# Kernel tuning notes

Hardware: AMD Instinct MI355X
Metric: run time of the kernel (lower is better)

The kernel has to match this reference:

```python
import jax, jax.numpy as jnp
import numpy as np

NUM_SINK = 8  # cfg.SINKHORN_ITERS


def _sinkhorn_log(c, log_a, log_b, lambd):
    # c: [M+1, N+1] augmented coupling scores (sinkhorn_unrolled: log_p = -c/lambd)
    log_p = -c / lambd
    for _ in range(NUM_SINK):  # fixed small unroll, matches num_sink
        log_p = log_p - (jax.nn.logsumexp(log_p, axis=-2, keepdims=True) - log_b[None, :])
        log_p = log_p - (jax.nn.logsumexp(log_p, axis=-1, keepdims=True) - log_a[:, None])
    return jnp.exp(log_p)


def setup_inputs() -> dict:
    key = jax.random.key(0)
    k1, k2 = jax.random.split(key)
    G, M, N, D = 128, 512, 512, 512
    return {
        "det_feats": jax.random.normal(k1, (G, N, D), dtype=jnp.float32),
        "tra_feats": jax.random.normal(k2, (G, M, D), dtype=jnp.float32),
        "alpha": jnp.ones((1,), dtype=jnp.float32),
        "eplison": jnp.zeros((1,), dtype=jnp.float32),
    }


def reference(det_feats, tra_feats, alpha, eplison):
    G, N, D = det_feats.shape
    M = tra_feats.shape[1]
    # cosine affinity per graph: [G, M, N]
    corr = jnp.einsum('gmd,gnd->gmn', tra_feats, det_feats)
    n1 = jnp.linalg.norm(tra_feats, axis=-1)  # [G, M]
    n2 = jnp.linalg.norm(det_feats, axis=-1)  # [G, N]
    affinity = corr / (n1[:, :, None] * n2[:, None, :])
    a = alpha[0]
    bins0 = jnp.broadcast_to(a, (G, M, 1)).astype(affinity.dtype)
    bins1 = jnp.broadcast_to(a, (G, 1, N)).astype(affinity.dtype)
    corner = jnp.broadcast_to(a, (G, 1, 1)).astype(affinity.dtype)
    couplings = jnp.concatenate([
        jnp.concatenate([affinity, bins0], axis=-1),
        jnp.concatenate([bins1, corner], axis=-1),
    ], axis=-2)  # [G, M+1, N+1]
    norm = 1.0 / (M + N)
    a_aug = jnp.full((M + 1,), norm, dtype=jnp.float32).at[-1].set(norm * N)
    b_aug = jnp.full((N + 1,), norm, dtype=jnp.float32).at[-1].set(norm * M)
    log_a = jnp.log(a_aug)
    log_b = jnp.log(b_aug)
    lambd = jnp.exp(eplison[0]) + 0.03
    pred = jax.vmap(lambda c: _sinkhorn_log(c, log_a, log_b, lambd))(couplings)
    return pred  # [G, M+1, N+1]
```

## Files before the change

kernel.cpp:

```cpp
#include <hip/hip_runtime.h>
#include <hip/hip_bf16.h>

#define G    128
#define MDIM 512
#define NDIM 512
#define DDIM 512
#define NORMC 0.0009765625f
#define BINW  0.5f
#define PW   516

using short8 = __attribute__((ext_vector_type(8))) short;
using short4v = __attribute__((ext_vector_type(4))) short;
using f32x4 = __attribute__((ext_vector_type(4))) float;

__device__ inline float bf2f(unsigned short u) {
    unsigned int x = ((unsigned int)u) << 16;
    return __builtin_bit_cast(float, x);
}
__device__ inline unsigned short f2bf(float f) {
    return __builtin_bit_cast(unsigned short, __float2bfloat16(f));
}
__device__ inline short4v cvt4(float4 f) {
    short4v r;
    r[0] = __builtin_bit_cast(short, __float2bfloat16(f.x));
    r[1] = __builtin_bit_cast(short, __float2bfloat16(f.y));
    r[2] = __builtin_bit_cast(short, __float2bfloat16(f.z));
    r[3] = __builtin_bit_cast(short, __float2bfloat16(f.w));
    return r;
}

__global__ __launch_bounds__(256)
void gt_gemm_kernel(const float* __restrict__ tra, const float* __restrict__ det,
                    const float* __restrict__ eps,
                    float* __restrict__ Koutf, unsigned short* __restrict__ Ke,
                    float* __restrict__ P1, int bfout)
{
    __shared__ short As[128 * 40];
    __shared__ short Bs[128 * 40];
    __shared__ float rnA[128];
    __shared__ float rnB[128];
    int bid = blockIdx.x;
    int xcd = bid & 7, slot = bid >> 3;
    int g = xcd * 16 + (slot >> 4);
    int tile = slot & 15;
    int tm = tile >> 2, tn = tile & 3;
    int t = threadIdx.x, lane = t & 63, wave = t >> 6;
    int wr = wave >> 1, wc = wave & 1;
    f32x4 acc[4][4] = {};
    const float* Abase = tra + (size_t)g * MDIM * DDIM + (size_t)(tm * 128) * DDIM;
    const float* Bbase = det + (size_t)g * NDIM * DDIM + (size_t)(tn * 128) * DDIM;
    int srow = t >> 3, scol = t & 7;
    float ssA[4] = {0.f, 0.f, 0.f, 0.f};
    float ssB[4] = {0.f, 0.f, 0.f, 0.f};

    for (int kt = 0; kt < 16; ++kt) {
        int k0 = kt * 32;
        #pragma unroll
        for (int p = 0; p < 4; ++p) {
            int row = p * 32 + srow;
            float4 a = *reinterpret_cast<const float4*>(Abase + (size_t)row * DDIM + k0 + scol * 4);
            float4 b = *reinterpret_cast<const float4*>(Bbase + (size_t)row * DDIM + k0 + scol * 4);
            ssA[p] += a.x*a.x + a.y*a.y + a.z*a.z + a.w*a.w;
            ssB[p] += b.x*b.x + b.y*b.y + b.z*b.z + b.w*b.w;
            *reinterpret_cast<short4v*>(&As[row * 40 + scol * 4]) = cvt4(a);
            *reinterpret_cast<short4v*>(&Bs[row * 40 + scol * 4]) = cvt4(b);
        }
        __syncthreads();
        short8 af[4], bfv[4];
        #pragma unroll
        for (int i = 0; i < 4; ++i) {
            int arow = wr * 64 + i * 16 + (lane & 15);
            af[i]  = *reinterpret_cast<const short8*>(&As[arow * 40 + (lane >> 4) * 8]);
            int brow = wc * 64 + i * 16 + (lane & 15);
            bfv[i] = *reinterpret_cast<const short8*>(&Bs[brow * 40 + (lane >> 4) * 8]);
        }
        #pragma unroll
        for (int i = 0; i < 4; ++i)
            #pragma unroll
            for (int j = 0; j < 4; ++j)
                acc[i][j] = __builtin_amdgcn_mfma_f32_16x16x32_bf16(af[i], bfv[j], acc[i][j], 0, 0, 0);
        __syncthreads();
    }

    #pragma unroll
    for (int p = 0; p < 4; ++p) {
        float a = ssA[p], b = ssB[p];
        a += __shfl_xor(a, 1); a += __shfl_xor(a, 2); a += __shfl_xor(a, 4);
        b += __shfl_xor(b, 1); b += __shfl_xor(b, 2); b += __shfl_xor(b, 4);
        if (scol == 0) { rnA[p * 32 + srow] = rsqrtf(a); rnB[p * 32 + srow] = rsqrtf(b); }
    }
    __syncthreads();

    float lam = __expf(eps[0]) + 0.03f;
    float nscale = -1.0f / lam;
    size_t kbase = (size_t)g << 18;
    size_t obase = (size_t)g * 263169;
    int r0v = (lane >> 4) * 4;
    int c0 = lane & 15;
    #pragma unroll
    for (int j = 0; j < 4; ++j) {
        int lcol = wc * 64 + j * 16 + c0;
        int colg = tn * 128 + lcol;
        float sc2 = nscale * rnB[lcol];
        float cacc = 0.f;
        #pragma unroll
        for (int i = 0; i < 4; ++i) {
            int lrow = wr * 64 + i * 16 + r0v;
            #pragma unroll
            for (int r = 0; r < 4; ++r) {
                float ev = __expf(acc[i][j][r] * rnA[lrow + r] * sc2);
                cacc += ev;
                int rowg = tm * 128 + lrow + r;
                if (bfout) Ke[kbase + (size_t)rowg * 512 + colg] = f2bf(ev);
                else       Koutf[obase + (size_t)rowg * 513 + colg] = ev;
            }
        }
        cacc += __shfl_down(cacc, 32);
        cacc += __shfl_down(cacc, 16);
        if (lane < 16)
            P1[(size_t)g * (8 * PW) + (size_t)(2 * tm + wr) * PW + tn * 128 + wc * 64 + j * 16 + lane] = cacc;
    }
}

template<bool BF16>
__global__ __launch_bounds__(256)
void gt_iter(const void* __restrict__ Kv,
             const float* __restrict__ alpha, const float* __restrict__ eps,
             const float* __restrict__ Pread, float* __restrict__ Pwrite,
             float* __restrict__ auOut, int first, int writeP)
{
    __shared__ float bv_s[512];
    __shared__ float colpart[4][512];
    __shared__ float rtmp[4];
    __shared__ float scal[1];
    int g = blockIdx.y, rb = blockIdx.x;
    int t = threadIdx.x, lane = t & 63, wv = t >> 6;
    float lam = __expf(eps[0]) + 0.03f;
    float val = __expf(-alpha[0] / lam);
    const float* Pg = Pread + (size_t)g * (8 * PW);
    float au512p = first ? 1.0f : Pg[513];
    float cs0 = 0.f, cs1 = 0.f;
    #pragma unroll
    for (int b = 0; b < 8; ++b) { cs0 += Pg[b * PW + t]; cs1 += Pg[b * PW + t + 256]; }
    float bv0 = NORMC / (cs0 + val * au512p);
    float bv1 = NORMC / (cs1 + val * au512p);
    bv_s[t] = bv0; bv_s[t + 256] = bv1;
    float sb = bv0 + bv1;
    #pragma unroll
    for (int off = 1; off < 64; off <<= 1) sb += __shfl_xor(sb, off);
    if (lane == 0) rtmp[wv] = sb;
    __syncthreads();
    if (t == 0) {
        float S_bv = rtmp[0] + rtmp[1] + rtmp[2] + rtmp[3];
        float S_au_prev;
        if (first) S_au_prev = 513.f;
        else { float s = 0.f; for (int b = 0; b < 8; ++b) s += Pg[b * PW + 512]; S_au_prev = s + au512p; }
        float bv512 = BINW / (val * S_au_prev);
        float au512n = BINW / (val * (S_bv + bv512));
        scal[0] = bv512;
        if (rb == 0) Pwrite[(size_t)g * (8 * PW) + 513] = au512n;
    }
    __syncthreads();
    float bv512 = scal[0];

    float bvr[8];
    #pragma unroll
    for (int k = 0; k < 8; ++k) bvr[k] = bv_s[lane * 8 + k];
    float colacc[8] = {};
    float suma = 0.f;
    const size_t RS = BF16 ? 512 : 513;
    size_t base = BF16 ? ((size_t)g << 18) : ((size_t)g * 263169);
    int rowbase = rb * 64;
    for (int rr = wv; rr < 64; rr += 4) {
        int r = rowbase + rr;
        float kv[8];
        if constexpr (BF16) {
            short8 x = *reinterpret_cast<const short8*>((const unsigned short*)Kv + base + (size_t)r * RS + lane * 8);
            #pragma unroll
            for (int k = 0; k < 8; ++k) kv[k] = bf2f((unsigned short)x[k]);
        } else {
            const float* p = (const float*)Kv + base + (size_t)r * RS + lane * 8;
            #pragma unroll
            for (int k = 0; k < 8; ++k) kv[k] = p[k];
        }
        float dot = 0.f;
        #pragma unroll
        for (int k = 0; k < 8; ++k) dot += kv[k] * bvr[k];
        #pragma unroll
        for (int off = 1; off < 64; off <<= 1) dot += __shfl_xor(dot, off);
        float au_r = NORMC / (dot + val * bv512);
        suma += au_r;
        #pragma unroll
        for (int k = 0; k < 8; ++k) colacc[k] += kv[k] * au_r;
        if (lane == 0) auOut[g * 512 + r] = au_r;
    }
    if (writeP) {
        #pragma unroll
        for (int k = 0; k < 8; ++k) colpart[wv][lane * 8 + k] = colacc[k];
        if (lane == 0) rtmp[wv] = suma;
        __syncthreads();
        float s0 = colpart[0][t] + colpart[1][t] + colpart[2][t] + colpart[3][t];
        float s1 = colpart[0][t + 256] + colpart[1][t + 256] + colpart[2][t + 256] + colpart[3][t + 256];
        float* Pw = Pwrite + (size_t)g * (8 * PW) + (size_t)rb * PW;
        Pw[t] = s0; Pw[t + 256] = s1;
        if (t == 0) Pw[512] = rtmp[0] + rtmp[1] + rtmp[2] + rtmp[3];
    }
}

template<bool BF16>
__global__ __launch_bounds__(256)
void gt_final(const void* Kv, const float* __restrict__ alpha, const float* __restrict__ eps,
              const float* __restrict__ P6, const float* __restrict__ P7,
              const float* __restrict__ au, float* out)
{
    __shared__ float bv_s[512];
    __shared__ float scal[2];
    int g = blockIdx.y, rb = blockIdx.x;
    int t = threadIdx.x, lane = t & 63, wv = t >> 6;
    float lam = __expf(eps[0]) + 0.03f;
    float val = __expf(-alpha[0] / lam);
    const float* Pg = P6 + (size_t)g * (8 * PW);
    float au512_6 = Pg[513];
    float cs0 = 0.f, cs1 = 0.f;
    #pragma unroll
    for (int b = 0; b < 8; ++b) { cs0 += Pg[b * PW + t]; cs1 += Pg[b * PW + t + 256]; }
    bv_s[t] = NORMC / (cs0 + val * au512_6);
    bv_s[t + 256] = NORMC / (cs1 + val * au512_6);
    if (t == 0) {
        float s = 0.f;
        for (int b = 0; b < 8; ++b) s += Pg[b * PW + 512];
        scal[0] = BINW / (val * (s + au512_6));
        scal[1] = P7[(size_t)g * (8 * PW) + 513];
    }
    __syncthreads();
    float bv512 = scal[0], au512_7 = scal[1];
    size_t base = BF16 ? ((size_t)g << 18) : ((size_t)g * 263169);
    size_t obase = (size_t)g * 263169;
    for (int rr = wv; rr < 64; rr += 4) {
        int r = rb * 64 + rr;
        float au_r = au[g * 512 + r];
        float* orow = out + obase + (size_t)r * 513;
        if constexpr (BF16) {
            const unsigned short* kr = (const unsigned short*)Kv + base + (size_t)r * 512;
            #pragma unroll
            for (int k = 0; k < 8; ++k) {
                int j = lane + 64 * k;
                orow[j] = bf2f(kr[j]) * au_r * bv_s[j];
            }
        } else {
            const float* kr = (const float*)Kv + base + (size_t)r * 513;
            #pragma unroll
            for (int k = 0; k < 8; ++k) {
                int j = lane + 64 * k;
                orow[j] = kr[j] * au_r * bv_s[j];
            }
        }
        if (lane == 0) orow[512] = val * au_r * bv512;
    }
    if (rb == 7) {
        float* brow = out + obase + (size_t)512 * 513;
        brow[t] = val * au512_7 * bv_s[t];
        brow[t + 256] = val * au512_7 * bv_s[t + 256];
        if (t == 0) brow[512] = val * au512_7 * bv512;
    }
}

extern "C" void kernel_launch(void* const* d_in, const int* in_sizes, int n_in,
                              void* d_out, int out_size, void* d_ws, size_t ws_size,
                              hipStream_t stream) {
    const float* det   = (const float*)d_in[0];
    const float* tra   = (const float*)d_in[1];
    const float* alpha = (const float*)d_in[2];
    const float* eps   = (const float*)d_in[3];
    float* out = (float*)d_out;

    float* P0 = (float*)d_ws;
    float* P1 = P0 + (size_t)G * 8 * PW;
    float* au = P1 + (size_t)G * 8 * PW;
    unsigned short* ke = (unsigned short*)(au + (size_t)G * 512);

    size_t smallBytes = ((size_t)2 * G * 8 * PW + (size_t)G * 512) * 4;
    bool fast = ws_size >= smallBytes + ((size_t)G << 19);

    gt_gemm_kernel<<<2048, 256, 0, stream>>>(tra, det, eps, out, ke, P1, fast ? 1 : 0);
    const void* K = fast ? (const void*)ke : (const void*)out;

    float* Pr = P1; float* Pw = P0;
    for (int it = 0; it < 8; ++it) {
        if (fast) gt_iter<true ><<<dim3(8, G), 256, 0, stream>>>(K, alpha, eps, Pr, Pw, au, it == 0 ? 1 : 0, it < 7 ? 1 : 0);
        else      gt_iter<false><<<dim3(8, G), 256, 0, stream>>>(K, alpha, eps, Pr, Pw, au, it == 0 ? 1 : 0, it < 7 ? 1 : 0);
        float* tmp = Pr; Pr = Pw; Pw = tmp;
    }
    if (fast) gt_final<true ><<<dim3(8, G), 256, 0, stream>>>(K, alpha, eps, P0, P1, au, out);
    else      gt_final<false><<<dim3(8, G), 256, 0, stream>>>(K, alpha, eps, P0, P1, au, out);
}
```

Measured before the change: 320.7 us.

## Pre-normalize and convert features to bf16 in a separate pass before GEMM

After: 311.6 us. 2.9% less time.

```diff
diff --git a/kernel.cpp b/kernel.cpp
--- a/kernel.cpp
+++ b/kernel.cpp
@@ -30,10 +30,109 @@
 }
 
 __global__ __launch_bounds__(256)
-void gt_gemm_kernel(const float* __restrict__ tra, const float* __restrict__ det,
+void gt_cvt_kernel(const float* __restrict__ tra, const float* __restrict__ det,
+                   unsigned short* __restrict__ trab, unsigned short* __restrict__ detb)
+{
+    int wave = threadIdx.x >> 6, lane = threadIdx.x & 63;
+    long row = (long)blockIdx.x * 4 + wave;
+    const long per = (long)G * MDIM;
+    const float* src; unsigned short* dst; long r;
+    if (row < per) { src = tra; dst = trab; r = row; }
+    else           { src = det; dst = detb; r = row - per; }
+    const float4* p = reinterpret_cast<const float4*>(src + r * DDIM);
+    float4 x0 = p[lane];
+    float4 x1 = p[lane + 64];
+    float s = x0.x*x0.x + x0.y*x0.y + x0.z*x0.z + x0.w*x0.w
+            + x1.x*x1.x + x1.y*x1.y + x1.z*x1.z + x1.w*x1.w;
+    #pragma unroll
+    for (int off = 1; off < 64; off <<= 1) s += __shfl_xor(s, off);
+    float rs = rsqrtf(s);
+    float4 y0 = make_float4(x0.x*rs, x0.y*rs, x0.z*rs, x0.w*rs);
+    float4 y1 = make_float4(x1.x*rs, x1.y*rs, x1.z*rs, x1.w*rs);
+    unsigned short* drow = dst + (size_t)r * 512;
+    *reinterpret_cast<short4v*>(drow + lane * 4)       = cvt4(y0);
+    *reinterpret_cast<short4v*>(drow + 256 + lane * 4) = cvt4(y1);
+}
+
+__global__ __launch_bounds__(256)
+void gt_gemm_bf16(const unsigned short* __restrict__ trab, const unsigned short* __restrict__ detb,
+                  const float* __restrict__ eps,
+                  unsigned short* __restrict__ Ke, float* __restrict__ P1)
+{
+    __shared__ short As[128 * 40];
+    __shared__ short Bs[128 * 40];
+    int bid = blockIdx.x;
+    int xcd = bid & 7, slot = bid >> 3;
+    int g = xcd * 16 + (slot >> 4);
+    int tile = slot & 15;
+    int tm = tile >> 2, tn = tile & 3;
+    int t = threadIdx.x, lane = t & 63, wave = t >> 6;
+    int wr = wave >> 1, wc = wave & 1;
+    f32x4 acc[4][4] = {};
+    const unsigned short* Ab = trab + ((size_t)g << 18) + (size_t)(tm * 128) * 512;
+    const unsigned short* Bb = detb + ((size_t)g << 18) + (size_t)(tn * 128) * 512;
+    int srow = t >> 2;
+    int sslot = t & 3;
+
+    for (int kt = 0; kt < 16; ++kt) {
+        int k0 = kt * 32;
+        #pragma unroll
+        for (int p = 0; p < 2; ++p) {
+            int row = p * 64 + srow;
+            short8 a = *reinterpret_cast<const short8*>(Ab + (size_t)row * 512 + k0 + sslot * 8);
+            short8 b = *reinterpret_cast<const short8*>(Bb + (size_t)row * 512 + k0 + sslot * 8);
+            *reinterpret_cast<short8*>(&As[row * 40 + sslot * 8]) = a;
+            *reinterpret_cast<short8*>(&Bs[row * 40 + sslot * 8]) = b;
+        }
+        __syncthreads();
+        short8 af[4], bfv[4];
+        #pragma unroll
+        for (int i = 0; i < 4; ++i) {
+            int arow = wr * 64 + i * 16 + (lane & 15);
+            af[i]  = *reinterpret_cast<const short8*>(&As[arow * 40 + (lane >> 4) * 8]);
+            int brow = wc * 64 + i * 16 + (lane & 15);
+            bfv[i] = *reinterpret_cast<const short8*>(&Bs[brow * 40 + (lane >> 4) * 8]);
+        }
+        #pragma unroll
+        for (int i = 0; i < 4; ++i)
+            #pragma unroll
+            for (int j = 0; j < 4; ++j)
+                acc[i][j] = __builtin_amdgcn_mfma_f32_16x16x32_bf16(af[i], bfv[j], acc[i][j], 0, 0, 0);
+        __syncthreads();
+    }
+
+    float lam = __expf(eps[0]) + 0.03f;
+    float nscale = -1.0f / lam;
+    size_t kbase = (size_t)g << 18;
+    int r0v = (lane >> 4) * 4;
+    int c0 = lane & 15;
+    #pragma unroll
+    for (int j = 0; j < 4; ++j) {
+        int lcol = wc * 64 + j * 16 + c0;
+        int colg = tn * 128 + lcol;
+        float cacc = 0.f;
+        #pragma unroll
+        for (int i = 0; i < 4; ++i) {
+            int lrow = wr * 64 + i * 16 + r0v;
+            #pragma unroll
+            for (int r = 0; r < 4; ++r) {
+                float ev = __expf(acc[i][j][r] * nscale);
+                cacc += ev;
+                int rowg = tm * 128 + lrow + r;
+                Ke[kbase + (size_t)rowg * 512 + colg] = f2bf(ev);
+            }
+        }
+        cacc += __shfl_down(cacc, 32);
+        cacc += __shfl_down(cacc, 16);
+        if (lane < 16)
+            P1[(size_t)g * (8 * PW) + (size_t)(2 * tm + wr) * PW + tn * 128 + wc * 64 + j * 16 + lane] = cacc;
+    }
+}
+
+__global__ __launch_bounds__(256)
+void gt_gemm_legacy(const float* __restrict__ tra, const float* __restrict__ det,
                     const float* __restrict__ eps,
-                    float* __restrict__ Koutf, unsigned short* __restrict__ Ke,
-                    float* __restrict__ P1, int bfout)
+                    float* __restrict__ Koutf, float* __restrict__ P1)
 {
     __shared__ short As[128 * 40];
     __shared__ short Bs[128 * 40];
@@ -93,7 +192,6 @@
 
     float lam = __expf(eps[0]) + 0.03f;
     float nscale = -1.0f / lam;
-    size_t kbase = (size_t)g << 18;
     size_t obase = (size_t)g * 263169;
     int r0v = (lane >> 4) * 4;
     int c0 = lane & 15;
@@ -111,8 +209,7 @@
                 float ev = __expf(acc[i][j][r] * rnA[lrow + r] * sc2);
                 cacc += ev;
                 int rowg = tm * 128 + lrow + r;
-                if (bfout) Ke[kbase + (size_t)rowg * 512 + colg] = f2bf(ev);
-                else       Koutf[obase + (size_t)rowg * 513 + colg] = ev;
+                Koutf[obase + (size_t)rowg * 513 + colg] = ev;
             }
         }
         cacc += __shfl_down(cacc, 32);
@@ -282,15 +379,24 @@
     size_t smallBytes = ((size_t)2 * G * 8 * PW + (size_t)G * 512) * 4;
     bool fast = ws_size >= smallBytes + ((size_t)G << 19);
 
-    gt_gemm_kernel<<<2048, 256, 0, stream>>>(tra, det, eps, out, ke, P1, fast ? 1 : 0);
-    const void* K = fast ? (const void*)ke : (const void*)out;
-
-    float* Pr = P1; float* Pw = P0;
-    for (int it = 0; it < 8; ++it) {
-        if (fast) gt_iter<true ><<<dim3(8, G), 256, 0, stream>>>(K, alpha, eps, Pr, Pw, au, it == 0 ? 1 : 0, it < 7 ? 1 : 0);
-        else      gt_iter<false><<<dim3(8, G), 256, 0, stream>>>(K, alpha, eps, Pr, Pw, au, it == 0 ? 1 : 0, it < 7 ? 1 : 0);
-        float* tmp = Pr; Pr = Pw; Pw = tmp;
-    }
-    if (fast) gt_final<true ><<<dim3(8, G), 256, 0, stream>>>(K, alpha, eps, P0, P1, au, out);
-    else      gt_final<false><<<dim3(8, G), 256, 0, stream>>>(K, alpha, eps, P0, P1, au, out);
-}
+    if (fast) {
+        unsigned short* trab = (unsigned short*)out;
+        unsigned short* detb = trab + ((size_t)G << 18);
+        gt_cvt_kernel<<<(2 * G * MDIM) / 4, 256, 0, stream>>>(tra, det, trab, detb);
+        gt_gemm_bf16<<<2048, 256, 0, stream>>>(trab, detb, eps, ke, P1);
+        float* Pr = P1; float* Pw = P0;
+        for (int it = 0; it < 8; ++it) {
+            gt_iter<true><<<dim3(8, G), 256, 0, stream>>>((const void*)ke, alpha, eps, Pr, Pw, au, it == 0 ? 1 : 0, it < 7 ? 1 : 0);
+            float* tmp = Pr; Pr = Pw; Pw = tmp;
+        }
+        gt_final<true><<<dim3(8, G), 256, 0, stream>>>((const void*)ke, alpha, eps, P0, P1, au, out);
+    } else {
+        gt_gemm_legacy<<<2048, 256, 0, stream>>>(tra, det, eps, out, P1);
+        float* Pr = P1; float* Pw = P0;
+        for (int it = 0; it < 8; ++it) {
+            gt_iter<false><<<dim3(8, G), 256, 0, stream>>>((const void*)out, alpha, eps, Pr, Pw, au, it == 0 ? 1 : 0, it < 7 ? 1 : 0);
+            float* tmp = Pr; Pr = Pw; Pw = tmp;
+        }
+        gt_final<false><<<dim3(8, G), 256, 0, stream>>>((const void*)out, alpha, eps, P0, P1, au, out);
+    }
+}
```

## Fuse final Sinkhorn output into last iteration and precompute row norms separately

Applied to the files above, without the earlier changes.

Measured after the change: 307.1 us. 1.04x faster.

```diff
diff --git a/kernel.cpp b/kernel.cpp
--- a/kernel.cpp
+++ b/kernel.cpp
@@ -30,7 +30,27 @@
 }
 
 __global__ __launch_bounds__(256)
+void gt_norms_kernel(const float* __restrict__ tra, const float* __restrict__ det,
+                     float* __restrict__ inv1, float* __restrict__ inv2) {
+    int wave = threadIdx.x >> 6;
+    int lane = threadIdx.x & 63;
+    long row = (long)blockIdx.x * 4 + wave;
+    const long per = (long)G * MDIM;
+    const float* src; float* dst; long r;
+    if (row < per) { src = tra; dst = inv1; r = row; }
+    else           { src = det; dst = inv2; r = row - per; }
+    const float4* p = reinterpret_cast<const float4*>(src + r * DDIM);
+    float4 x0 = p[lane];
+    float4 x1 = p[lane + 64];
+    float s = x0.x*x0.x + x0.y*x0.y + x0.z*x0.z + x0.w*x0.w
+            + x1.x*x1.x + x1.y*x1.y + x1.z*x1.z + x1.w*x1.w;
+    for (int off = 32; off; off >>= 1) s += __shfl_down(s, off);
+    if (lane == 0) dst[r] = rsqrtf(s);
+}
+
+__global__ __launch_bounds__(256)
 void gt_gemm_kernel(const float* __restrict__ tra, const float* __restrict__ det,
+                    const float* __restrict__ inv1, const float* __restrict__ inv2,
                     const float* __restrict__ eps,
                     float* __restrict__ Koutf, unsigned short* __restrict__ Ke,
                     float* __restrict__ P1, int bfout)
@@ -46,12 +66,12 @@
     int tm = tile >> 2, tn = tile & 3;
     int t = threadIdx.x, lane = t & 63, wave = t >> 6;
     int wr = wave >> 1, wc = wave & 1;
+    if (t < 128) rnA[t] = inv1[g * 512 + tm * 128 + t];
+    else         rnB[t - 128] = inv2[g * 512 + tn * 128 + (t - 128)];
     f32x4 acc[4][4] = {};
     const float* Abase = tra + (size_t)g * MDIM * DDIM + (size_t)(tm * 128) * DDIM;
     const float* Bbase = det + (size_t)g * NDIM * DDIM + (size_t)(tn * 128) * DDIM;
     int srow = t >> 3, scol = t & 7;
-    float ssA[4] = {0.f, 0.f, 0.f, 0.f};
-    float ssB[4] = {0.f, 0.f, 0.f, 0.f};
 
     for (int kt = 0; kt < 16; ++kt) {
         int k0 = kt * 32;
@@ -60,8 +80,6 @@
             int row = p * 32 + srow;
             float4 a = *reinterpret_cast<const float4*>(Abase + (size_t)row * DDIM + k0 + scol * 4);
             float4 b = *reinterpret_cast<const float4*>(Bbase + (size_t)row * DDIM + k0 + scol * 4);
-            ssA[p] += a.x*a.x + a.y*a.y + a.z*a.z + a.w*a.w;
-            ssB[p] += b.x*b.x + b.y*b.y + b.z*b.z + b.w*b.w;
             *reinterpret_cast<short4v*>(&As[row * 40 + scol * 4]) = cvt4(a);
             *reinterpret_cast<short4v*>(&Bs[row * 40 + scol * 4]) = cvt4(b);
         }
@@ -81,15 +99,6 @@
                 acc[i][j] = __builtin_amdgcn_mfma_f32_16x16x32_bf16(af[i], bfv[j], acc[i][j], 0, 0, 0);
         __syncthreads();
     }
-
-    #pragma unroll
-    for (int p = 0; p < 4; ++p) {
-        float a = ssA[p], b = ssB[p];
-        a += __shfl_xor(a, 1); a += __shfl_xor(a, 2); a += __shfl_xor(a, 4);
-        b += __shfl_xor(b, 1); b += __shfl_xor(b, 2); b += __shfl_xor(b, 4);
-        if (scol == 0) { rnA[p * 32 + srow] = rsqrtf(a); rnB[p * 32 + srow] = rsqrtf(b); }
-    }
-    __syncthreads();
 
     float lam = __expf(eps[0]) + 0.03f;
     float nscale = -1.0f / lam;
@@ -122,43 +131,50 @@
     }
 }
 
-template<bool BF16>
-__global__ __launch_bounds__(256)
+template<bool BF16, bool LAST>
+__global__ __launch_bounds__(512)
 void gt_iter(const void* __restrict__ Kv,
              const float* __restrict__ alpha, const float* __restrict__ eps,
              const float* __restrict__ Pread, float* __restrict__ Pwrite,
-             float* __restrict__ auOut, int first, int writeP)
+             float* __restrict__ outp, int first, int writeP)
 {
     __shared__ float bv_s[512];
-    __shared__ float colpart[4][512];
-    __shared__ float rtmp[4];
-    __shared__ float scal[1];
-    int g = blockIdx.y, rb = blockIdx.x;
+    __shared__ float colpart[8][512];
+    __shared__ float rtmp[8];
+    __shared__ float scal[2];
+    int id = blockIdx.x;
+    int xcd = id & 7;
+    int q = id >> 3;
+    int gi = q >> 3;
+    int rb = q & 7;
+    int g = xcd * 16 + gi;
     int t = threadIdx.x, lane = t & 63, wv = t >> 6;
     float lam = __expf(eps[0]) + 0.03f;
     float val = __expf(-alpha[0] / lam);
     const float* Pg = Pread + (size_t)g * (8 * PW);
     float au512p = first ? 1.0f : Pg[513];
-    float cs0 = 0.f, cs1 = 0.f;
-    #pragma unroll
-    for (int b = 0; b < 8; ++b) { cs0 += Pg[b * PW + t]; cs1 += Pg[b * PW + t + 256]; }
-    float bv0 = NORMC / (cs0 + val * au512p);
-    float bv1 = NORMC / (cs1 + val * au512p);
-    bv_s[t] = bv0; bv_s[t + 256] = bv1;
-    float sb = bv0 + bv1;
+    float cs = 0.f;
+    #pragma unroll
+    for (int b = 0; b < 8; ++b) cs += Pg[b * PW + t];
+    float bvt = NORMC / (cs + val * au512p);
+    bv_s[t] = bvt;
+    float sb = bvt;
     #pragma unroll
     for (int off = 1; off < 64; off <<= 1) sb += __shfl_xor(sb, off);
     if (lane == 0) rtmp[wv] = sb;
     __syncthreads();
     if (t == 0) {
-        float S_bv = rtmp[0] + rtmp[1] + rtmp[2] + rtmp[3];
+        float S_bv = 0.f;
+        #pragma unroll
+        for (int w = 0; w < 8; ++w) S_bv += rtmp[w];
         float S_au_prev;
         if (first) S_au_prev = 513.f;
         else { float s = 0.f; for (int b = 0; b < 8; ++b) s += Pg[b * PW + 512]; S_au_prev = s + au512p; }
         float bv512 = BINW / (val * S_au_prev);
         float au512n = BINW / (val * (S_bv + bv512));
         scal[0] = bv512;
-        if (rb == 0) Pwrite[(size_t)g * (8 * PW) + 513] = au512n;
+        scal[1] = au512n;
+        if (!LAST && rb == 0) Pwrite[(size_t)g * (8 * PW) + 513] = au512n;
     }
     __syncthreads();
     float bv512 = scal[0];
@@ -170,8 +186,9 @@
     float suma = 0.f;
     const size_t RS = BF16 ? 512 : 513;
     size_t base = BF16 ? ((size_t)g << 18) : ((size_t)g * 263169);
+    size_t obase = (size_t)g * 263169;
     int rowbase = rb * 64;
-    for (int rr = wv; rr < 64; rr += 4) {
+    for (int rr = wv; rr < 64; rr += 8) {
         int r = rowbase + rr;
         float kv[8];
         if constexpr (BF16) {
@@ -189,79 +206,46 @@
         #pragma unroll
         for (int off = 1; off < 64; off <<= 1) dot += __shfl_xor(dot, off);
         float au_r = NORMC / (dot + val * bv512);
-        suma += au_r;
-        #pragma unroll
-        for (int k = 0; k < 8; ++k) colacc[k] += kv[k] * au_r;
-        if (lane == 0) auOut[g * 512 + r] = au_r;
-    }
-    if (writeP) {
+        if constexpr (LAST) {
+            float* orow = outp + obase + (size_t)r * 513;
+            f32x4 o0, o1;
+            #pragma unroll
+            for (int k = 0; k < 4; ++k) {
+                o0[k] = kv[k] * au_r * bvr[k];
+                o1[k] = kv[4 + k] * au_r * bvr[4 + k];
+            }
+            *reinterpret_cast<f32x4*>(orow + lane * 8)     = o0;
+            *reinterpret_cast<f32x4*>(orow + lane * 8 + 4) = o1;
+            if (lane == 0) orow[512] = val * au_r * bv512;
+        } else {
+            suma += au_r;
+            #pragma unroll
+            for (int k = 0; k < 8; ++k) colacc[k] += kv[k] * au_r;
+        }
+    }
+    if constexpr (LAST) {
+        if (rb == 7) {
+            float au512n = scal[1];
+            float* brow = outp + obase + (size_t)512 * 513;
+            brow[t] = val * au512n * bv_s[t];
+            if (t == 0) brow[512] = val * au512n * bv512;
+        }
+    } else if (writeP) {
         #pragma unroll
         for (int k = 0; k < 8; ++k) colpart[wv][lane * 8 + k] = colacc[k];
         if (lane == 0) rtmp[wv] = suma;
         __syncthreads();
-        float s0 = colpart[0][t] + colpart[1][t] + colpart[2][t] + colpart[3][t];
-        float s1 = colpart[0][t + 256] + colpart[1][t + 256] + colpart[2][t + 256] + colpart[3][t + 256];
+        float s0 = 0.f;
+        #pragma unroll
+        for (int w = 0; w < 8; ++w) s0 += colpart[w][t];
         float* Pw = Pwrite + (size_t)g * (8 * PW) + (size_t)rb * PW;
-        Pw[t] = s0; Pw[t + 256] = s1;
-        if (t == 0) Pw[512] = rtmp[0] + rtmp[1] + rtmp[2] + rtmp[3];
-    }
-}
-
-template<bool BF16>
-__global__ __launch_bounds__(256)
-void gt_final(const void* Kv, const float* __restrict__ alpha, const float* __restrict__ eps,
-              const float* __restrict__ P6, const float* __restrict__ P7,
-              const float* __restrict__ au, float* out)
-{
-    __shared__ float bv_s[512];
-    __shared__ float scal[2];
-    int g = blockIdx.y, rb = blockIdx.x;
-    int t = threadIdx.x, lane = t & 63, wv = t >> 6;
-    float lam = __expf(eps[0]) + 0.03f;
-    float val = __expf(-alpha[0] / lam);
-    const float* Pg = P6 + (size_t)g * (8 * PW);
-    float au512_6 = Pg[513];
-    float cs0 = 0.f, cs1 = 0.f;
-    #pragma unroll
-    for (int b = 0; b < 8; ++b) { cs0 += Pg[b * PW + t]; cs1 += Pg[b * PW + t + 256]; }
-    bv_s[t] = NORMC / (cs0 + val * au512_6);
-    bv_s[t + 256] = NORMC / (cs1 + val * au512_6);
-    if (t == 0) {
-        float s = 0.f;
-        for (int b = 0; b < 8; ++b) s += Pg[b * PW + 512];
-        scal[0] = BINW / (val * (s + au512_6));
-        scal[1] = P7[(size_t)g * (8 * PW) + 513];
-    }
-    __syncthreads();
-    float bv512 = scal[0], au512_7 = scal[1];
-    size_t base = BF16 ? ((size_t)g << 18) : ((size_t)g * 263169);
-    size_t obase = (size_t)g * 263169;
-    for (int rr = wv; rr < 64; rr += 4) {
-        int r = rb * 64 + rr;
-        float au_r = au[g * 512 + r];
-        float* orow = out + obase + (size_t)r * 513;
-        if constexpr (BF16) {
-            const unsigned short* kr = (const unsigned short*)Kv + base + (size_t)r * 512;
-            #pragma unroll
-            for (int k = 0; k < 8; ++k) {
-                int j = lane + 64 * k;
-                orow[j] = bf2f(kr[j]) * au_r * bv_s[j];
-            }
-        } else {
-            const float* kr = (const float*)Kv + base + (size_t)r * 513;
-            #pragma unroll
-            for (int k = 0; k < 8; ++k) {
-                int j = lane + 64 * k;
-                orow[j] = kr[j] * au_r * bv_s[j];
-            }
-        }
-        if (lane == 0) orow[512] = val * au_r * bv512;
-    }
-    if (rb == 7) {
-        float* brow = out + obase + (size_t)512 * 513;
-        brow[t] = val * au512_7 * bv_s[t];
-        brow[t + 256] = val * au512_7 * bv_s[t + 256];
-        if (t == 0) brow[512] = val * au512_7 * bv512;
+        Pw[t] = s0;
+        if (t == 0) {
+            float ss = 0.f;
+            #pragma unroll
+            for (int w = 0; w < 8; ++w) ss += rtmp[w];
+            Pw[512] = ss;
+        }
     }
 }
 
@@ -274,23 +258,31 @@
     const float* eps   = (const float*)d_in[3];
     float* out = (float*)d_out;
 
-    float* P0 = (float*)d_ws;
+    float* inv1 = (float*)d_ws;
+    float* inv2 = inv1 + (size_t)G * 512;
+    float* P0 = inv2 + (size_t)G * 512;
     float* P1 = P0 + (size_t)G * 8 * PW;
-    float* au = P1 + (size_t)G * 8 * PW;
-    unsigned short* ke = (unsigned short*)(au + (size_t)G * 512);
-
-    size_t smallBytes = ((size_t)2 * G * 8 * PW + (size_t)G * 512) * 4;
+    unsigned short* ke = (unsigned short*)(P1 + (size_t)G * 8 * PW);
+
+    size_t smallBytes = ((size_t)2 * G * 512 + (size_t)2 * G * 8 * PW) * 4;
     bool fast = ws_size >= smallBytes + ((size_t)G << 19);
 
-    gt_gemm_kernel<<<2048, 256, 0, stream>>>(tra, det, eps, out, ke, P1, fast ? 1 : 0);
-    const void* K = fast ? (const void*)ke : (const void*)out;
-
-    float* Pr = P1; float* Pw = P0;
-    for (int it = 0; it < 8; ++it) {
-        if (fast) gt_iter<true ><<<dim3(8, G), 256, 0, stream>>>(K, alpha, eps, Pr, Pw, au, it == 0 ? 1 : 0, it < 7 ? 1 : 0);
-        else      gt_iter<false><<<dim3(8, G), 256, 0, stream>>>(K, alpha, eps, Pr, Pw, au, it == 0 ? 1 : 0, it < 7 ? 1 : 0);
-        float* tmp = Pr; Pr = Pw; Pw = tmp;
-    }
-    if (fast) gt_final<true ><<<dim3(8, G), 256, 0, stream>>>(K, alpha, eps, P0, P1, au, out);
-    else      gt_final<false><<<dim3(8, G), 256, 0, stream>>>(K, alpha, eps, P0, P1, au, out);
-}
+    gt_norms_kernel<<<(2 * G * MDIM) / 4, 256, 0, stream>>>(tra, det, inv1, inv2);
+    if (fast) {
+        gt_gemm_kernel<<<2048, 256, 0, stream>>>(tra, det, inv1, inv2, eps, nullptr, ke, P1, 1);
+        float* Pr = P1; float* Pw = P0;
+        for (int it = 0; it < 7; ++it) {
+            gt_iter<true, false><<<1024, 512, 0, stream>>>((const void*)ke, alpha, eps, Pr, Pw, nullptr, it == 0 ? 1 : 0, 1);
+            float* tmp = Pr; Pr = Pw; Pw = tmp;
+        }
+        gt_iter<true, true><<<1024, 512, 0, stream>>>((const void*)ke, alpha, eps, Pr, Pw, out, 0, 0);
+    } else {
+        gt_gemm_kernel<<<2048, 256, 0, stream>>>(tra, det, inv1, inv2, eps, out, nullptr, P1, 0);
+        float* Pr = P1; float* Pw = P0;
+        for (int it = 0; it < 7; ++it) {
+            gt_iter<false, false><<<1024, 512, 0, stream>>>((const void*)out, alpha, eps, Pr, Pw, nullptr, it == 0 ? 1 : 0, 1);
+            float* tmp = Pr; Pr = Pw; Pw = tmp;
+        }
+        gt_iter<false, true><<<1024, 512, 0, stream>>>((const void*)out, alpha, eps, Pr, Pw, out, 0, 0);
+    }
+}
```
